# Kernel optimization log

Measured on AMD Instinct MI355X. Metric: run time of the kernel, lower is better.

## Reference

```python
import jax, jax.numpy as jnp
import numpy as np

TOP_K = 4
NORM_TOPK_PROB = True


def setup_inputs() -> dict:
    key = jax.random.key(0)
    kx, kg, k1, k3, k2 = jax.random.split(key, 5)
    B, S, H, I, E = 1, 2048, 1024, 512, 16
    scale = 0.02
    return {
        "hidden_states": jax.random.normal(kx, (B, S, H), jnp.float32),
        "gate_w": jax.random.normal(kg, (E, H), jnp.float32) * scale,   # router Linear weight [E,H]
        "w1": jax.random.normal(k1, (E, I, H), jnp.float32) * scale,    # intermediateDense per expert
        "w3": jax.random.normal(k3, (E, I, H), jnp.float32) * scale,    # intermediateDense2 per expert
        "w2": jax.random.normal(k2, (E, H, I), jnp.float32) * scale,    # outputDense per expert
    }


def reference(hidden_states, gate_w, w1, w3, w2):
    B, S, H = hidden_states.shape
    x = hidden_states.reshape(-1, H)                    # [T,H]
    T = x.shape[0]
    E = gate_w.shape[0]

    # Router: softmax in fp32, top-k, optional renorm (norm_topk_prob=True)
    router_logits = x @ gate_w.T                        # [T,E]
    probs = jax.nn.softmax(router_logits.astype(jnp.float32), axis=-1)
    routing_weights, selected = jax.lax.top_k(probs, TOP_K)   # [T,K], [T,K]
    if NORM_TOPK_PROB:
        routing_weights = routing_weights / routing_weights.sum(-1, keepdims=True)
    routing_weights = routing_weights.astype(x.dtype)

    # Dense per-token expert-weight matrix: zero for unselected experts, so
    # the combine below computes exactly the torch gather->FFN->index_add math.
    w = jnp.zeros((T, E), x.dtype).at[jnp.arange(T)[:, None], selected].add(routing_weights)

    # Gated SiLU FFN for every expert, combined with routing weights.
    h1 = jnp.einsum('th,eih->tei', x, w1)               # [T,E,I]
    h3 = jnp.einsum('th,eih->tei', x, w3)               # [T,E,I]
    act = jax.nn.silu(h1) * h3                          # [T,E,I]
    out = jnp.einsum('tei,ehi,te->th', act, w2, w)      # [T,H]
    return out.reshape(B, S, H)
```

## Files before the change

### kernel.cpp

```cpp
#include <hip/hip_runtime.h>
#include <hip/hip_bf16.h>

#define T 2048
#define H 1024
#define IDIM 512
#define E 16
#define TOPK 4
#define NPAIR (T * TOPK)

typedef short bf16x8 __attribute__((ext_vector_type(8)));
typedef float f32x4 __attribute__((ext_vector_type(4)));

static __device__ __forceinline__ unsigned short f2bf(float f) {
    union { float f; unsigned int u; } v; v.f = f;
    unsigned int r = (v.u + 0x7FFFu + ((v.u >> 16) & 1u)) >> 16;
    return (unsigned short)r;
}
static __device__ __forceinline__ float bf2f(unsigned short s) {
    union { unsigned int u; float f; } v; v.u = ((unsigned int)s) << 16;
    return v.f;
}

static __device__ __forceinline__ void async_ld16(const unsigned short* g, unsigned short* l) {
    __builtin_amdgcn_global_load_lds((const __attribute__((address_space(1))) void*)g,
                                     (__attribute__((address_space(3))) void*)l, 16, 0, 0);
}

__global__ __launch_bounds__(256) void cvt3_kernel(
    const float* __restrict__ w1, const float* __restrict__ w3, const float* __restrict__ w2,
    unsigned short* __restrict__ d1, unsigned short* __restrict__ d3, unsigned short* __restrict__ d2)
{
    const int n4 = (E * IDIM * H) / 4;
    int region = blockIdx.x >> 11;
    int bid = blockIdx.x & 2047;
    const float* src = (region == 0) ? w1 : (region == 1) ? w3 : w2;
    unsigned short* dst = (region == 0) ? d1 : (region == 1) ? d3 : d2;
    int i = bid * 256 + threadIdx.x;
    const int stride = 2048 * 256;
#pragma unroll 4
    for (; i < n4; i += stride) {
        float4 v = ((const float4*)src)[i];
        ushort4 o;
        o.x = f2bf(v.x); o.y = f2bf(v.y); o.z = f2bf(v.z); o.w = f2bf(v.w);
        ((ushort4*)dst)[i] = o;
    }
}

__global__ __launch_bounds__(256) void router_kernel(
    const float* __restrict__ x, const float* __restrict__ gw,
    int* __restrict__ topk_idx, float* __restrict__ topk_w,
    unsigned short* __restrict__ xb)
{
    int tok = blockIdx.x * 4 + (threadIdx.x >> 6);
    int lane = threadIdx.x & 63;
    if (tok >= T) return;
    const float4* xt4 = (const float4*)(x + (size_t)tok * H);
    float4 xr[4];
#pragma unroll
    for (int j = 0; j < 4; ++j) xr[j] = xt4[lane + j * 64];
    ushort4* xbt = (ushort4*)(xb + (size_t)tok * H);
#pragma unroll
    for (int j = 0; j < 4; ++j) {
        ushort4 o;
        o.x = f2bf(xr[j].x); o.y = f2bf(xr[j].y);
        o.z = f2bf(xr[j].z); o.w = f2bf(xr[j].w);
        xbt[lane + j * 64] = o;
    }
    float logits[E];
#pragma unroll
    for (int e = 0; e < E; ++e) {
        const float4* ge4 = (const float4*)(gw + (size_t)e * H);
        float acc = 0.f;
#pragma unroll
        for (int j = 0; j < 4; ++j) {
            float4 g = ge4[lane + j * 64];
            acc += xr[j].x * g.x + xr[j].y * g.y + xr[j].z * g.z + xr[j].w * g.w;
        }
#pragma unroll
        for (int off = 32; off; off >>= 1) acc += __shfl_xor(acc, off, 64);
        logits[e] = acc;
    }
    if (lane == 0) {
        float m = logits[0];
#pragma unroll
        for (int e = 1; e < E; ++e) m = fmaxf(m, logits[e]);
        float p[E];
#pragma unroll
        for (int e = 0; e < E; ++e) p[e] = __expf(logits[e] - m);
        int sel[TOPK]; float wv[TOPK]; float tot = 0.f;
#pragma unroll
        for (int k = 0; k < TOPK; ++k) {
            int best = 0; float bv = -1.f;
#pragma unroll
            for (int e = 0; e < E; ++e) { if (p[e] > bv) { bv = p[e]; best = e; } }
            sel[k] = best; wv[k] = bv; tot += bv; p[best] = -2.f;
        }
#pragma unroll
        for (int k = 0; k < TOPK; ++k) {
            topk_idx[tok * TOPK + k] = sel[k];
            topk_w[tok * TOPK + k] = wv[k] / tot;
        }
    }
}

__global__ __launch_bounds__(256) void hist_kernel(
    const int* __restrict__ topk_idx, int* __restrict__ offsets)
{
    __shared__ int h[4][E];
    int tid = threadIdx.x, wave = tid >> 6;
    if (tid < 4 * E) ((int*)h)[tid] = 0;
    __syncthreads();
    for (int i = tid; i < NPAIR; i += 256) atomicAdd(&h[wave][topk_idx[i]], 1);
    __syncthreads();
    if (tid == 0) {
        int s = 0;
#pragma unroll
        for (int e = 0; e < E; ++e) {
            offsets[e] = s;
            s += h[0][e] + h[1][e] + h[2][e] + h[3][e];
        }
        offsets[E] = s;
    }
}

__global__ __launch_bounds__(256) void scatter_kernel(
    const int* __restrict__ topk_idx,
    const int* __restrict__ offsets, int* __restrict__ cursor,
    int* __restrict__ pair_token, int* __restrict__ inv_pos)
{
    __shared__ int lh[E];
    __shared__ int base[E];
    int tid = threadIdx.x;
    int i = blockIdx.x * 256 + tid;
    if (tid < E) lh[tid] = 0;
    __syncthreads();
    int e = topk_idx[i];
    int lr = atomicAdd(&lh[e], 1);
    __syncthreads();
    if (tid < E) base[tid] = atomicAdd(&cursor[tid], lh[tid]);
    __syncthreads();
    int pos = offsets[e] + base[e] + lr;
    pair_token[pos] = i >> 2;
    inv_pos[i] = pos;
}


__global__ __launch_bounds__(256, 5) void gemm_a_kernel(
    const unsigned short* __restrict__ xb,
    const unsigned short* __restrict__ wb1,
    const unsigned short* __restrict__ wb3,
    const int* __restrict__ offsets,
    const int* __restrict__ pair_token,
    unsigned short* __restrict__ act)
{
    __shared__ unsigned short Xs[2][128 * 32];
    __shared__ unsigned short W1s[2][64 * 32];
    __shared__ unsigned short W3s[2][64 * 32];

    int bid = blockIdx.x;
    int xcd = bid & 7, s0 = bid >> 3;
    int yz = xcd * 16 + (s0 >> 4);
    int e = yz >> 3;
    int n0 = (yz & 7) * 64;
    int t0 = (s0 & 15) * 128;

    int beg = offsets[e];
    int cnt = offsets[e + 1] - beg;
    if (t0 >= cnt) return;

    int tid = threadIdx.x;
    int wave = tid >> 6, lane = tid & 63;

    const unsigned short* xg[2];
#pragma unroll
    for (int i = 0; i < 2; ++i) {
        int slot = wave * 128 + i * 64 + lane;
        int g = slot >> 3, sp = (slot & 7) ^ (g & 7);
        int row = g * 2 + (sp >> 2), c = sp & 3;
        int r = t0 + row; if (r >= cnt) r = cnt - 1;
        xg[i] = xb + (size_t)pair_token[beg + r] * H + c * 8;
    }
    const unsigned short* w1g;
    const unsigned short* w3g;
    {
        int slot = wave * 64 + lane;
        int g = slot >> 3, sp = (slot & 7) ^ (g & 7);
        int row = g * 2 + (sp >> 2), c = sp & 3;
        size_t off = (size_t)e * IDIM * H + (size_t)(n0 + row) * H + c * 8;
        w1g = wb1 + off;
        w3g = wb3 + off;
    }

    int wr = wave >> 1, wc = wave & 1;
    int lm = lane & 15, lq = lane >> 4;

    f32x4 acc1[4][2], acc3[4][2];
#pragma unroll
    for (int mi = 0; mi < 4; ++mi)
#pragma unroll
        for (int nj = 0; nj < 2; ++nj) {
            acc1[mi][nj] = (f32x4){0.f, 0.f, 0.f, 0.f};
            acc3[mi][nj] = (f32x4){0.f, 0.f, 0.f, 0.f};
        }

    int aoff[4], boff[2];
#pragma unroll
    for (int mi = 0; mi < 4; ++mi) {
        int m = wr * 64 + mi * 16 + lm;
        int g = m >> 1;
        aoff[mi] = g * 64 + (((lq + ((m & 1) << 2)) ^ (g & 7)) << 3);
    }
#pragma unroll
    for (int nj = 0; nj < 2; ++nj) {
        int n = wc * 32 + nj * 16 + lm;
        int g = n >> 1;
        boff[nj] = g * 64 + (((lq + ((n & 1) << 2)) ^ (g & 7)) << 3);
    }

#pragma unroll
    for (int i = 0; i < 2; ++i) async_ld16(xg[i], &Xs[0][(wave * 128 + i * 64) * 8]);
    async_ld16(w1g, &W1s[0][wave * 512]);
    async_ld16(w3g, &W3s[0][wave * 512]);

    const int NK = H / 32;
    for (int kk = 0; kk < NK; ++kk) {
        int cur = kk & 1;
        __syncthreads();
        if (kk + 1 < NK) {
            int nxt = cur ^ 1;
            int k1 = (kk + 1) * 32;
#pragma unroll
            for (int i = 0; i < 2; ++i) async_ld16(xg[i] + k1, &Xs[nxt][(wave * 128 + i * 64) * 8]);
            async_ld16(w1g + k1, &W1s[nxt][wave * 512]);
            async_ld16(w3g + k1, &W3s[nxt][wave * 512]);
        }
        bf16x8 af[4], b1[2], b3[2];
#pragma unroll
        for (int mi = 0; mi < 4; ++mi) af[mi] = *(const bf16x8*)&Xs[cur][aoff[mi]];
#pragma unroll
        for (int nj = 0; nj < 2; ++nj) {
            b1[nj] = *(const bf16x8*)&W1s[cur][boff[nj]];
            b3[nj] = *(const bf16x8*)&W3s[cur][boff[nj]];
        }
#pragma unroll
        for (int mi = 0; mi < 4; ++mi)
#pragma unroll
            for (int nj = 0; nj < 2; ++nj) {
                acc1[mi][nj] = __builtin_amdgcn_mfma_f32_16x16x32_bf16(af[mi], b1[nj], acc1[mi][nj], 0, 0, 0);
                acc3[mi][nj] = __builtin_amdgcn_mfma_f32_16x16x32_bf16(af[mi], b3[nj], acc3[mi][nj], 0, 0, 0);
            }
    }
#pragma unroll
    for (int mi = 0; mi < 4; ++mi) {
#pragma unroll
        for (int r = 0; r < 4; ++r) {
            int trow = t0 + wr * 64 + mi * 16 + lq * 4 + r;
            if (trow < cnt) {
                size_t base = (size_t)(beg + trow) * IDIM + n0 + wc * 32 + lm;
#pragma unroll
                for (int nj = 0; nj < 2; ++nj) {
                    float h1 = acc1[mi][nj][r];
                    float sg = h1 / (1.f + __expf(-h1));
                    act[base + nj * 16] = f2bf(sg * acc3[mi][nj][r]);
                }
            }
        }
    }
}

__global__ __launch_bounds__(256, 5) void gemm_b_kernel(
    const unsigned short* __restrict__ act,
    const unsigned short* __restrict__ wb2,
    const int* __restrict__ offsets,
    unsigned short* __restrict__ outp)
{
    __shared__ unsigned short As[2][128 * 32];
    __shared__ unsigned short W2s[2][64 * 32];

    int bid = blockIdx.x;
    int xcd = bid & 7, s0 = bid >> 3;
    int yz = xcd * 32 + (s0 >> 4);
    int e = yz >> 4;
    int h0 = (yz & 15) * 64;
    int t0 = (s0 & 15) * 128;

    int beg = offsets[e];
    int cnt = offsets[e + 1] - beg;
    if (t0 >= cnt) return;

    int tid = threadIdx.x;
    int wave = tid >> 6, lane = tid & 63;

    const unsigned short* ag[2];
#pragma unroll
    for (int i = 0; i < 2; ++i) {
        int slot = wave * 128 + i * 64 + lane;
        int g = slot >> 3, sp = (slot & 7) ^ (g & 7);
        int row = g * 2 + (sp >> 2), c = sp & 3;
        int ar = beg + t0 + row; if (ar > NPAIR - 1) ar = NPAIR - 1;
        ag[i] = act + (size_t)ar * IDIM + c * 8;
    }
    const unsigned short* w2g;
    {
        int slot = wave * 64 + lane;
        int g = slot >> 3, sp = (slot & 7) ^ (g & 7);
        int row = g * 2 + (sp >> 2), c = sp & 3;
        w2g = wb2 + (size_t)e * H * IDIM + (size_t)(h0 + row) * IDIM + c * 8;
    }

    int wr = wave >> 1, wc = wave & 1;
    int lm = lane & 15, lq = lane >> 4;

    f32x4 acc[4][2];
#pragma unroll
    for (int mi = 0; mi < 4; ++mi)
#pragma unroll
        for (int nj = 0; nj < 2; ++nj) acc[mi][nj] = (f32x4){0.f, 0.f, 0.f, 0.f};

    int aoff[4], boff[2];
#pragma unroll
    for (int mi = 0; mi < 4; ++mi) {
        int m = wr * 64 + mi * 16 + lm;
        int g = m >> 1;
        aoff[mi] = g * 64 + (((lq + ((m & 1) << 2)) ^ (g & 7)) << 3);
    }
#pragma unroll
    for (int nj = 0; nj < 2; ++nj) {
        int n = wc * 32 + nj * 16 + lm;
        int g = n >> 1;
        boff[nj] = g * 64 + (((lq + ((n & 1) << 2)) ^ (g & 7)) << 3);
    }

#pragma unroll
    for (int i = 0; i < 2; ++i) async_ld16(ag[i], &As[0][(wave * 128 + i * 64) * 8]);
    async_ld16(w2g, &W2s[0][wave * 512]);

    const int NK = IDIM / 32;
    for (int kk = 0; kk < NK; ++kk) {
        int cur = kk & 1;
        __syncthreads();
        if (kk + 1 < NK) {
            int nxt = cur ^ 1;
            int k1 = (kk + 1) * 32;
#pragma unroll
            for (int i = 0; i < 2; ++i) async_ld16(ag[i] + k1, &As[nxt][(wave * 128 + i * 64) * 8]);
            async_ld16(w2g + k1, &W2s[nxt][wave * 512]);
        }
        bf16x8 af[4], bfr[2];
#pragma unroll
        for (int mi = 0; mi < 4; ++mi) af[mi] = *(const bf16x8*)&As[cur][aoff[mi]];
#pragma unroll
        for (int nj = 0; nj < 2; ++nj) bfr[nj] = *(const bf16x8*)&W2s[cur][boff[nj]];
#pragma unroll
        for (int mi = 0; mi < 4; ++mi)
#pragma unroll
            for (int nj = 0; nj < 2; ++nj)
                acc[mi][nj] = __builtin_amdgcn_mfma_f32_16x16x32_bf16(af[mi], bfr[nj], acc[mi][nj], 0, 0, 0);
    }
#pragma unroll
    for (int mi = 0; mi < 4; ++mi) {
#pragma unroll
        for (int r = 0; r < 4; ++r) {
            int trow = t0 + wr * 64 + mi * 16 + lq * 4 + r;
            if (trow < cnt) {
                unsigned short* orow = outp + (size_t)(beg + trow) * H + h0 + wc * 32 + lm;
#pragma unroll
                for (int nj = 0; nj < 2; ++nj) orow[nj * 16] = f2bf(acc[mi][nj][r]);
            }
        }
    }
}

__global__ __launch_bounds__(256) void combine_kernel(
    const unsigned short* __restrict__ outp, const int* __restrict__ inv_pos,
    const float* __restrict__ topk_w, float* __restrict__ out)
{
    int gid = blockIdx.x * 256 + threadIdx.x;
    int t = gid >> 8;
    int c4 = gid & 255;
    float4 a = make_float4(0.f, 0.f, 0.f, 0.f);
#pragma unroll
    for (int k = 0; k < TOPK; ++k) {
        int pos = inv_pos[t * TOPK + k];
        float w = topk_w[t * TOPK + k];
        ushort4 v = ((const ushort4*)(outp + (size_t)pos * H))[c4];
        a.x += w * bf2f(v.x); a.y += w * bf2f(v.y);
        a.z += w * bf2f(v.z); a.w += w * bf2f(v.w);
    }
    *(float4*)(out + (size_t)t * H + c4 * 4) = a;
}

extern "C" void kernel_launch(void* const* d_in, const int* in_sizes, int n_in,
                              void* d_out, int out_size, void* d_ws, size_t ws_size,
                              hipStream_t stream)
{
    const float* x  = (const float*)d_in[0];
    const float* gw = (const float*)d_in[1];
    const float* w1 = (const float*)d_in[2];
    const float* w3 = (const float*)d_in[3];
    const float* w2 = (const float*)d_in[4];
    float* out = (float*)d_out;

    char* ws = (char*)d_ws;
    int*   cursor     = (int*)(ws + 64);
    int*   offsets    = (int*)(ws + 128);
    int*   topk_idx   = (int*)(ws + 1024);
    float* topk_w     = (float*)(ws + 33792);
    int*   pair_token = (int*)(ws + 66560);
    int*   inv_pos    = (int*)(ws + 99328);
    unsigned short* xb  = (unsigned short*)(ws + 262144);
    unsigned short* wb1 = (unsigned short*)(ws + 8388608);
    unsigned short* wb3 = (unsigned short*)(ws + 25165824);
    unsigned short* wb2 = (unsigned short*)(ws + 41943040);
    unsigned short* act = (unsigned short*)(ws + 58720256);
    unsigned short* outp = (unsigned short*)(ws + 8388608);

    hipMemsetAsync(ws, 0, 256, stream);

    router_kernel<<<T / 4, 256, 0, stream>>>(x, gw, topk_idx, topk_w, xb);
    hist_kernel<<<1, 256, 0, stream>>>(topk_idx, offsets);
    scatter_kernel<<<NPAIR / 256, 256, 0, stream>>>(topk_idx, offsets, cursor,
                                                    pair_token, inv_pos);

    cvt3_kernel<<<3 * 2048, 256, 0, stream>>>(w1, w3, w2, wb1, wb3, wb2);

    gemm_a_kernel<<<2048, 256, 0, stream>>>(xb, wb1, wb3, offsets, pair_token, act);
    gemm_b_kernel<<<4096, 256, 0, stream>>>(act, wb2, offsets, outp);
    combine_kernel<<<(T * H / 4) / 256, 256, 0, stream>>>(outp, inv_pos, topk_w, out);
}
```

Measured before the change: 229.6 us.

## Deepen async LDS prefetch pipelines in both expert GEMM kernels

Replaces the double-buffered k-loop in gemm_a with a 4-stage ring (three tiles in flight) and gemm_b with a 3-stage ring, using explicit vmcnt waits plus raw s_barrier instead of __syncthreads. This keeps more global_load_lds transfers outstanding so load latency is hidden behind MFMA work. The price is more LDS per block, and the occupancy hints drop to 2 blocks/SM for gemm_a and 4 for gemm_b. Correctness depends on the hand-counted vmcnt values matching the number of loads each stage issues.

Result: slower. 234.8 us (+2.2%).

```diff
diff --git a/kernel.cpp b/kernel.cpp
--- a/kernel.cpp
+++ b/kernel.cpp
@@ -145,7 +145,28 @@
 }
 
 
-__global__ __launch_bounds__(256, 5) void gemm_a_kernel(
+static __device__ __forceinline__ void ga_compute(
+    const unsigned short* xs, const unsigned short* w1s, const unsigned short* w3s,
+    const int* aoff, const int* boff, f32x4 acc1[4][2], f32x4 acc3[4][2])
+{
+    bf16x8 af[4], b1[2], b3[2];
+#pragma unroll
+    for (int mi = 0; mi < 4; ++mi) af[mi] = *(const bf16x8*)&xs[aoff[mi]];
+#pragma unroll
+    for (int nj = 0; nj < 2; ++nj) {
+        b1[nj] = *(const bf16x8*)&w1s[boff[nj]];
+        b3[nj] = *(const bf16x8*)&w3s[boff[nj]];
+    }
+#pragma unroll
+    for (int mi = 0; mi < 4; ++mi)
+#pragma unroll
+        for (int nj = 0; nj < 2; ++nj) {
+            acc1[mi][nj] = __builtin_amdgcn_mfma_f32_16x16x32_bf16(af[mi], b1[nj], acc1[mi][nj], 0, 0, 0);
+            acc3[mi][nj] = __builtin_amdgcn_mfma_f32_16x16x32_bf16(af[mi], b3[nj], acc3[mi][nj], 0, 0, 0);
+        }
+}
+
+__global__ __launch_bounds__(256, 2) void gemm_a_kernel(
     const unsigned short* __restrict__ xb,
     const unsigned short* __restrict__ wb1,
     const unsigned short* __restrict__ wb3,
@@ -153,9 +174,9 @@
     const int* __restrict__ pair_token,
     unsigned short* __restrict__ act)
 {
-    __shared__ unsigned short Xs[2][128 * 32];
-    __shared__ unsigned short W1s[2][64 * 32];
-    __shared__ unsigned short W3s[2][64 * 32];
+    __shared__ unsigned short Xs[4][128 * 32];
+    __shared__ unsigned short W1s[4][64 * 32];
+    __shared__ unsigned short W3s[4][64 * 32];
 
     int bid = blockIdx.x;
     int xcd = bid & 7, s0 = bid >> 3;
@@ -217,39 +238,41 @@
         boff[nj] = g * 64 + (((lq + ((n & 1) << 2)) ^ (g & 7)) << 3);
     }
 
-#pragma unroll
-    for (int i = 0; i < 2; ++i) async_ld16(xg[i], &Xs[0][(wave * 128 + i * 64) * 8]);
-    async_ld16(w1g, &W1s[0][wave * 512]);
-    async_ld16(w3g, &W3s[0][wave * 512]);
+    auto stage = [&](int buf, int kt) {
+        int k1 = kt * 32;
+#pragma unroll
+        for (int i = 0; i < 2; ++i)
+            async_ld16(xg[i] + k1, &Xs[buf][(wave * 128 + i * 64) * 8]);
+        async_ld16(w1g + k1, &W1s[buf][wave * 512]);
+        async_ld16(w3g + k1, &W3s[buf][wave * 512]);
+    };
+
+    stage(0, 0); stage(1, 1); stage(2, 2);
 
     const int NK = H / 32;
-    for (int kk = 0; kk < NK; ++kk) {
-        int cur = kk & 1;
-        __syncthreads();
-        if (kk + 1 < NK) {
-            int nxt = cur ^ 1;
-            int k1 = (kk + 1) * 32;
-#pragma unroll
-            for (int i = 0; i < 2; ++i) async_ld16(xg[i] + k1, &Xs[nxt][(wave * 128 + i * 64) * 8]);
-            async_ld16(w1g + k1, &W1s[nxt][wave * 512]);
-            async_ld16(w3g + k1, &W3s[nxt][wave * 512]);
-        }
-        bf16x8 af[4], b1[2], b3[2];
-#pragma unroll
-        for (int mi = 0; mi < 4; ++mi) af[mi] = *(const bf16x8*)&Xs[cur][aoff[mi]];
-#pragma unroll
-        for (int nj = 0; nj < 2; ++nj) {
-            b1[nj] = *(const bf16x8*)&W1s[cur][boff[nj]];
-            b3[nj] = *(const bf16x8*)&W3s[cur][boff[nj]];
-        }
-#pragma unroll
-        for (int mi = 0; mi < 4; ++mi)
-#pragma unroll
-            for (int nj = 0; nj < 2; ++nj) {
-                acc1[mi][nj] = __builtin_amdgcn_mfma_f32_16x16x32_bf16(af[mi], b1[nj], acc1[mi][nj], 0, 0, 0);
-                acc3[mi][nj] = __builtin_amdgcn_mfma_f32_16x16x32_bf16(af[mi], b3[nj], acc3[mi][nj], 0, 0, 0);
-            }
-    }
+    for (int kk = 0; kk < NK - 2; ++kk) {
+        int cur = kk & 3;
+        asm volatile("s_waitcnt vmcnt(8)" ::: "memory");
+        __builtin_amdgcn_s_barrier();
+        __builtin_amdgcn_sched_barrier(0);
+        if (kk + 3 < NK) stage((kk + 3) & 3, kk + 3);
+        ga_compute(Xs[cur], W1s[cur], W3s[cur], aoff, boff, acc1, acc3);
+    }
+    {
+        int cur = (NK - 2) & 3;
+        asm volatile("s_waitcnt vmcnt(4)" ::: "memory");
+        __builtin_amdgcn_s_barrier();
+        __builtin_amdgcn_sched_barrier(0);
+        ga_compute(Xs[cur], W1s[cur], W3s[cur], aoff, boff, acc1, acc3);
+    }
+    {
+        int cur = (NK - 1) & 3;
+        asm volatile("s_waitcnt vmcnt(0)" ::: "memory");
+        __builtin_amdgcn_s_barrier();
+        __builtin_amdgcn_sched_barrier(0);
+        ga_compute(Xs[cur], W1s[cur], W3s[cur], aoff, boff, acc1, acc3);
+    }
+
 #pragma unroll
     for (int mi = 0; mi < 4; ++mi) {
 #pragma unroll
@@ -268,14 +291,30 @@
     }
 }
 
-__global__ __launch_bounds__(256, 5) void gemm_b_kernel(
+static __device__ __forceinline__ void gb_compute(
+    const unsigned short* as, const unsigned short* w2s,
+    const int* aoff, const int* boff, f32x4 acc[4][2])
+{
+    bf16x8 af[4], bfr[2];
+#pragma unroll
+    for (int mi = 0; mi < 4; ++mi) af[mi] = *(const bf16x8*)&as[aoff[mi]];
+#pragma unroll
+    for (int nj = 0; nj < 2; ++nj) bfr[nj] = *(const bf16x8*)&w2s[boff[nj]];
+#pragma unroll
+    for (int mi = 0; mi < 4; ++mi)
+#pragma unroll
+        for (int nj = 0; nj < 2; ++nj)
+            acc[mi][nj] = __builtin_amdgcn_mfma_f32_16x16x32_bf16(af[mi], bfr[nj], acc[mi][nj], 0, 0, 0);
+}
+
+__global__ __launch_bounds__(256, 4) void gemm_b_kernel(
     const unsigned short* __restrict__ act,
     const unsigned short* __restrict__ wb2,
     const int* __restrict__ offsets,
     unsigned short* __restrict__ outp)
 {
-    __shared__ unsigned short As[2][128 * 32];
-    __shared__ unsigned short W2s[2][64 * 32];
+    __shared__ unsigned short As[3][128 * 32];
+    __shared__ unsigned short W2s[3][64 * 32];
 
     int bid = blockIdx.x;
     int xcd = bid & 7, s0 = bid >> 3;
@@ -331,32 +370,34 @@
         boff[nj] = g * 64 + (((lq + ((n & 1) << 2)) ^ (g & 7)) << 3);
     }
 
-#pragma unroll
-    for (int i = 0; i < 2; ++i) async_ld16(ag[i], &As[0][(wave * 128 + i * 64) * 8]);
-    async_ld16(w2g, &W2s[0][wave * 512]);
+    auto stage = [&](int buf, int kt) {
+        int k1 = kt * 32;
+#pragma unroll
+        for (int i = 0; i < 2; ++i)
+            async_ld16(ag[i] + k1, &As[buf][(wave * 128 + i * 64) * 8]);
+        async_ld16(w2g + k1, &W2s[buf][wave * 512]);
+    };
+
+    stage(0, 0); stage(1, 1);
 
     const int NK = IDIM / 32;
-    for (int kk = 0; kk < NK; ++kk) {
-        int cur = kk & 1;
-        __syncthreads();
-        if (kk + 1 < NK) {
-            int nxt = cur ^ 1;
-            int k1 = (kk + 1) * 32;
-#pragma unroll
-            for (int i = 0; i < 2; ++i) async_ld16(ag[i] + k1, &As[nxt][(wave * 128 + i * 64) * 8]);
-            async_ld16(w2g + k1, &W2s[nxt][wave * 512]);
-        }
-        bf16x8 af[4], bfr[2];
-#pragma unroll
-        for (int mi = 0; mi < 4; ++mi) af[mi] = *(const bf16x8*)&As[cur][aoff[mi]];
-#pragma unroll
-        for (int nj = 0; nj < 2; ++nj) bfr[nj] = *(const bf16x8*)&W2s[cur][boff[nj]];
-#pragma unroll
-        for (int mi = 0; mi < 4; ++mi)
-#pragma unroll
-            for (int nj = 0; nj < 2; ++nj)
-                acc[mi][nj] = __builtin_amdgcn_mfma_f32_16x16x32_bf16(af[mi], bfr[nj], acc[mi][nj], 0, 0, 0);
-    }
+    int cur = 0, pre = 2;
+    for (int kk = 0; kk < NK - 1; ++kk) {
+        asm volatile("s_waitcnt vmcnt(3)" ::: "memory");
+        __builtin_amdgcn_s_barrier();
+        __builtin_amdgcn_sched_barrier(0);
+        if (kk + 2 < NK) stage(pre, kk + 2);
+        gb_compute(As[cur], W2s[cur], aoff, boff, acc);
+        cur = (cur == 2) ? 0 : cur + 1;
+        pre = (pre == 2) ? 0 : pre + 1;
+    }
+    {
+        asm volatile("s_waitcnt vmcnt(0)" ::: "memory");
+        __builtin_amdgcn_s_barrier();
+        __builtin_amdgcn_sched_barrier(0);
+        gb_compute(As[cur], W2s[cur], aoff, boff, acc);
+    }
+
 #pragma unroll
     for (int mi = 0; mi < 4; ++mi) {
 #pragma unroll
```

## Fuse weight conversion with router, fold histogram, scatter-add output in GEMM B

Applied to the files above, without the earlier changes.

Merges the weight-conversion and router kernels into one launch and builds the expert histogram with global atomics inside the router, leaving a tiny scan kernel in place of the histogram kernel. GEMM B now multiplies by the routing weight and atomically adds fp32 results straight into the zeroed output, which removes the bf16 intermediate buffer and the combine kernel. The cost is an extra memset of the output and contended fp32 atomics, up to four per output element, plus non-deterministic summation order.

Result: slower. 328.4 us (+43.0%).

```diff
diff --git a/kernel.cpp b/kernel.cpp
--- a/kernel.cpp
+++ b/kernel.cpp
@@ -26,32 +26,32 @@
                                      (__attribute__((address_space(3))) void*)l, 16, 0, 0);
 }
 
-__global__ __launch_bounds__(256) void cvt3_kernel(
+__global__ __launch_bounds__(256) void prep_kernel(
     const float* __restrict__ w1, const float* __restrict__ w3, const float* __restrict__ w2,
-    unsigned short* __restrict__ d1, unsigned short* __restrict__ d3, unsigned short* __restrict__ d2)
-{
-    const int n4 = (E * IDIM * H) / 4;
-    int region = blockIdx.x >> 11;
-    int bid = blockIdx.x & 2047;
-    const float* src = (region == 0) ? w1 : (region == 1) ? w3 : w2;
-    unsigned short* dst = (region == 0) ? d1 : (region == 1) ? d3 : d2;
-    int i = bid * 256 + threadIdx.x;
-    const int stride = 2048 * 256;
-#pragma unroll 4
-    for (; i < n4; i += stride) {
-        float4 v = ((const float4*)src)[i];
-        ushort4 o;
-        o.x = f2bf(v.x); o.y = f2bf(v.y); o.z = f2bf(v.z); o.w = f2bf(v.w);
-        ((ushort4*)dst)[i] = o;
-    }
-}
-
-__global__ __launch_bounds__(256) void router_kernel(
+    unsigned short* __restrict__ d1, unsigned short* __restrict__ d3, unsigned short* __restrict__ d2,
     const float* __restrict__ x, const float* __restrict__ gw,
     int* __restrict__ topk_idx, float* __restrict__ topk_w,
-    unsigned short* __restrict__ xb)
-{
-    int tok = blockIdx.x * 4 + (threadIdx.x >> 6);
+    unsigned short* __restrict__ xb, int* __restrict__ ghist)
+{
+    if (blockIdx.x < 3 * 2048) {
+        const int n4 = (E * IDIM * H) / 4;
+        int region = blockIdx.x >> 11;
+        int bid = blockIdx.x & 2047;
+        const float* src = (region == 0) ? w1 : (region == 1) ? w3 : w2;
+        unsigned short* dst = (region == 0) ? d1 : (region == 1) ? d3 : d2;
+        int i = bid * 256 + threadIdx.x;
+        const int stride = 2048 * 256;
+#pragma unroll 4
+        for (; i < n4; i += stride) {
+            float4 v = ((const float4*)src)[i];
+            ushort4 o;
+            o.x = f2bf(v.x); o.y = f2bf(v.y); o.z = f2bf(v.z); o.w = f2bf(v.w);
+            ((ushort4*)dst)[i] = o;
+        }
+        return;
+    }
+    int rbid = blockIdx.x - 3 * 2048;
+    int tok = rbid * 4 + (threadIdx.x >> 6);
     int lane = threadIdx.x & 63;
     if (tok >= T) return;
     const float4* xt4 = (const float4*)(x + (size_t)tok * H);
@@ -99,34 +99,26 @@
         for (int k = 0; k < TOPK; ++k) {
             topk_idx[tok * TOPK + k] = sel[k];
             topk_w[tok * TOPK + k] = wv[k] / tot;
-        }
-    }
-}
-
-__global__ __launch_bounds__(256) void hist_kernel(
-    const int* __restrict__ topk_idx, int* __restrict__ offsets)
-{
-    __shared__ int h[4][E];
-    int tid = threadIdx.x, wave = tid >> 6;
-    if (tid < 4 * E) ((int*)h)[tid] = 0;
-    __syncthreads();
-    for (int i = tid; i < NPAIR; i += 256) atomicAdd(&h[wave][topk_idx[i]], 1);
-    __syncthreads();
-    if (tid == 0) {
+            atomicAdd(&ghist[sel[k]], 1);
+        }
+    }
+}
+
+__global__ __launch_bounds__(64) void scan_kernel(
+    const int* __restrict__ ghist, int* __restrict__ offsets)
+{
+    if (threadIdx.x == 0) {
         int s = 0;
 #pragma unroll
-        for (int e = 0; e < E; ++e) {
-            offsets[e] = s;
-            s += h[0][e] + h[1][e] + h[2][e] + h[3][e];
-        }
+        for (int e = 0; e < E; ++e) { offsets[e] = s; s += ghist[e]; }
         offsets[E] = s;
     }
 }
 
 __global__ __launch_bounds__(256) void scatter_kernel(
-    const int* __restrict__ topk_idx,
+    const int* __restrict__ topk_idx, const float* __restrict__ topk_w,
     const int* __restrict__ offsets, int* __restrict__ cursor,
-    int* __restrict__ pair_token, int* __restrict__ inv_pos)
+    int* __restrict__ pair_token, float* __restrict__ pair_w)
 {
     __shared__ int lh[E];
     __shared__ int base[E];
@@ -141,7 +133,7 @@
     __syncthreads();
     int pos = offsets[e] + base[e] + lr;
     pair_token[pos] = i >> 2;
-    inv_pos[i] = pos;
+    pair_w[pos] = topk_w[i];
 }
 
 
@@ -272,7 +264,9 @@
     const unsigned short* __restrict__ act,
     const unsigned short* __restrict__ wb2,
     const int* __restrict__ offsets,
-    unsigned short* __restrict__ outp)
+    const int* __restrict__ pair_token,
+    const float* __restrict__ pair_w,
+    float* __restrict__ out)
 {
     __shared__ unsigned short As[2][128 * 32];
     __shared__ unsigned short W2s[2][64 * 32];
@@ -363,31 +357,15 @@
         for (int r = 0; r < 4; ++r) {
             int trow = t0 + wr * 64 + mi * 16 + lq * 4 + r;
             if (trow < cnt) {
-                unsigned short* orow = outp + (size_t)(beg + trow) * H + h0 + wc * 32 + lm;
-#pragma unroll
-                for (int nj = 0; nj < 2; ++nj) orow[nj * 16] = f2bf(acc[mi][nj][r]);
+                int p = beg + trow;
+                int tok = pair_token[p];
+                float wgt = pair_w[p];
+                float* orow = out + (size_t)tok * H + h0 + wc * 32 + lm;
+                atomicAdd(&orow[0],  wgt * acc[mi][0][r]);
+                atomicAdd(&orow[16], wgt * acc[mi][1][r]);
             }
         }
     }
-}
-
-__global__ __launch_bounds__(256) void combine_kernel(
-    const unsigned short* __restrict__ outp, const int* __restrict__ inv_pos,
-    const float* __restrict__ topk_w, float* __restrict__ out)
-{
-    int gid = blockIdx.x * 256 + threadIdx.x;
-    int t = gid >> 8;
-    int c4 = gid & 255;
-    float4 a = make_float4(0.f, 0.f, 0.f, 0.f);
-#pragma unroll
-    for (int k = 0; k < TOPK; ++k) {
-        int pos = inv_pos[t * TOPK + k];
-        float w = topk_w[t * TOPK + k];
-        ushort4 v = ((const ushort4*)(outp + (size_t)pos * H))[c4];
-        a.x += w * bf2f(v.x); a.y += w * bf2f(v.y);
-        a.z += w * bf2f(v.z); a.w += w * bf2f(v.w);
-    }
-    *(float4*)(out + (size_t)t * H + c4 * 4) = a;
 }
 
 extern "C" void kernel_launch(void* const* d_in, const int* in_sizes, int n_in,
@@ -402,29 +380,28 @@
     float* out = (float*)d_out;
 
     char* ws = (char*)d_ws;
+    int*   ghist      = (int*)(ws + 0);
     int*   cursor     = (int*)(ws + 64);
     int*   offsets    = (int*)(ws + 128);
     int*   topk_idx   = (int*)(ws + 1024);
     float* topk_w     = (float*)(ws + 33792);
     int*   pair_token = (int*)(ws + 66560);
-    int*   inv_pos    = (int*)(ws + 99328);
+    float* pair_w     = (float*)(ws + 99328);
     unsigned short* xb  = (unsigned short*)(ws + 262144);
     unsigned short* wb1 = (unsigned short*)(ws + 8388608);
     unsigned short* wb3 = (unsigned short*)(ws + 25165824);
     unsigned short* wb2 = (unsigned short*)(ws + 41943040);
     unsigned short* act = (unsigned short*)(ws + 58720256);
-    unsigned short* outp = (unsigned short*)(ws + 8388608);
 
     hipMemsetAsync(ws, 0, 256, stream);
-
-    router_kernel<<<T / 4, 256, 0, stream>>>(x, gw, topk_idx, topk_w, xb);
-    hist_kernel<<<1, 256, 0, stream>>>(topk_idx, offsets);
-    scatter_kernel<<<NPAIR / 256, 256, 0, stream>>>(topk_idx, offsets, cursor,
-                                                    pair_token, inv_pos);
-
-    cvt3_kernel<<<3 * 2048, 256, 0, stream>>>(w1, w3, w2, wb1, wb3, wb2);
+    hipMemsetAsync(out, 0, (size_t)T * H * sizeof(float), stream);
+
+    prep_kernel<<<3 * 2048 + T / 4, 256, 0, stream>>>(
+        w1, w3, w2, wb1, wb3, wb2, x, gw, topk_idx, topk_w, xb, ghist);
+    scan_kernel<<<1, 64, 0, stream>>>(ghist, offsets);
+    scatter_kernel<<<NPAIR / 256, 256, 0, stream>>>(topk_idx, topk_w, offsets, cursor,
+                                                    pair_token, pair_w);
 
     gemm_a_kernel<<<2048, 256, 0, stream>>>(xb, wb1, wb3, offsets, pair_token, act);
-    gemm_b_kernel<<<4096, 256, 0, stream>>>(act, wb2, offsets, outp);
-    combine_kernel<<<(T * H / 4) / 256, 256, 0, stream>>>(outp, inv_pos, topk_w, out);
-}
+    gemm_b_kernel<<<4096, 256, 0, stream>>>(act, wb2, offsets, pair_token, pair_w, out);
+}
```

## Fuse fp32-to-bf16 weight conversion into expert GEMM tile loads

Applied to the files above, without the earlier changes.

Drops the separate kernel that converted all expert weights to bf16 in workspace. Both expert GEMMs now read fp32 weights straight from global memory into registers, convert them to bf16 and write them to LDS, prefetching one k-tile ahead. The token tile shrinks from 128 to 64 rows and the grids double, with occupancy hints adjusted. This removes a full pass of weight read and write traffic, but each expert's fp32 weights are now re-read by more token tiles at twice the bytes, and the synchronous register staging replaces the asynchronous global-to-LDS path for the weights.

Result: slower. 248.8 us (+8.4%).

```diff
diff --git a/kernel.cpp b/kernel.cpp
--- a/kernel.cpp
+++ b/kernel.cpp
@@ -24,26 +24,6 @@
 static __device__ __forceinline__ void async_ld16(const unsigned short* g, unsigned short* l) {
     __builtin_amdgcn_global_load_lds((const __attribute__((address_space(1))) void*)g,
                                      (__attribute__((address_space(3))) void*)l, 16, 0, 0);
-}
-
-__global__ __launch_bounds__(256) void cvt3_kernel(
-    const float* __restrict__ w1, const float* __restrict__ w3, const float* __restrict__ w2,
-    unsigned short* __restrict__ d1, unsigned short* __restrict__ d3, unsigned short* __restrict__ d2)
-{
-    const int n4 = (E * IDIM * H) / 4;
-    int region = blockIdx.x >> 11;
-    int bid = blockIdx.x & 2047;
-    const float* src = (region == 0) ? w1 : (region == 1) ? w3 : w2;
-    unsigned short* dst = (region == 0) ? d1 : (region == 1) ? d3 : d2;
-    int i = bid * 256 + threadIdx.x;
-    const int stride = 2048 * 256;
-#pragma unroll 4
-    for (; i < n4; i += stride) {
-        float4 v = ((const float4*)src)[i];
-        ushort4 o;
-        o.x = f2bf(v.x); o.y = f2bf(v.y); o.z = f2bf(v.z); o.w = f2bf(v.w);
-        ((ushort4*)dst)[i] = o;
-    }
 }
 
 __global__ __launch_bounds__(256) void router_kernel(
@@ -145,24 +125,24 @@
 }
 
 
-__global__ __launch_bounds__(256, 5) void gemm_a_kernel(
+__global__ __launch_bounds__(256, 4) void gemm_a_kernel(
     const unsigned short* __restrict__ xb,
-    const unsigned short* __restrict__ wb1,
-    const unsigned short* __restrict__ wb3,
+    const float* __restrict__ w1,
+    const float* __restrict__ w3,
     const int* __restrict__ offsets,
     const int* __restrict__ pair_token,
     unsigned short* __restrict__ act)
 {
-    __shared__ unsigned short Xs[2][128 * 32];
+    __shared__ unsigned short Xs[2][64 * 32];
     __shared__ unsigned short W1s[2][64 * 32];
     __shared__ unsigned short W3s[2][64 * 32];
 
     int bid = blockIdx.x;
     int xcd = bid & 7, s0 = bid >> 3;
-    int yz = xcd * 16 + (s0 >> 4);
+    int yz = xcd * 16 + (s0 >> 5);
     int e = yz >> 3;
     int n0 = (yz & 7) * 64;
-    int t0 = (s0 & 15) * 128;
+    int t0 = (s0 & 31) * 64;
 
     int beg = offsets[e];
     int cnt = offsets[e + 1] - beg;
@@ -171,42 +151,31 @@
     int tid = threadIdx.x;
     int wave = tid >> 6, lane = tid & 63;
 
-    const unsigned short* xg[2];
-#pragma unroll
-    for (int i = 0; i < 2; ++i) {
-        int slot = wave * 128 + i * 64 + lane;
-        int g = slot >> 3, sp = (slot & 7) ^ (g & 7);
-        int row = g * 2 + (sp >> 2), c = sp & 3;
-        int r = t0 + row; if (r >= cnt) r = cnt - 1;
-        xg[i] = xb + (size_t)pair_token[beg + r] * H + c * 8;
-    }
-    const unsigned short* w1g;
-    const unsigned short* w3g;
-    {
-        int slot = wave * 64 + lane;
-        int g = slot >> 3, sp = (slot & 7) ^ (g & 7);
-        int row = g * 2 + (sp >> 2), c = sp & 3;
-        size_t off = (size_t)e * IDIM * H + (size_t)(n0 + row) * H + c * 8;
-        w1g = wb1 + off;
-        w3g = wb3 + off;
-    }
+    int sg = tid >> 3, sp = (tid & 7) ^ (sg & 7);
+    int srow = sg * 2 + (sp >> 2), sc = sp & 3;
+
+    int r = t0 + srow; if (r >= cnt) r = cnt - 1;
+    const unsigned short* xg = xb + (size_t)pair_token[beg + r] * H + sc * 8;
+
+    const float* w1g = w1 + (size_t)e * IDIM * H + (size_t)(n0 + srow) * H + sc * 8;
+    const float* w3g = w3 + (size_t)e * IDIM * H + (size_t)(n0 + srow) * H + sc * 8;
 
     int wr = wave >> 1, wc = wave & 1;
     int lm = lane & 15, lq = lane >> 4;
 
-    f32x4 acc1[4][2], acc3[4][2];
-#pragma unroll
-    for (int mi = 0; mi < 4; ++mi)
+    f32x4 acc1[2][2], acc3[2][2];
+#pragma unroll
+    for (int mi = 0; mi < 2; ++mi)
 #pragma unroll
         for (int nj = 0; nj < 2; ++nj) {
             acc1[mi][nj] = (f32x4){0.f, 0.f, 0.f, 0.f};
             acc3[mi][nj] = (f32x4){0.f, 0.f, 0.f, 0.f};
         }
 
-    int aoff[4], boff[2];
-#pragma unroll
-    for (int mi = 0; mi < 4; ++mi) {
-        int m = wr * 64 + mi * 16 + lm;
+    int aoff[2], boff[2];
+#pragma unroll
+    for (int mi = 0; mi < 2; ++mi) {
+        int m = wr * 32 + mi * 16 + lm;
         int g = m >> 1;
         aoff[mi] = g * 64 + (((lq + ((m & 1) << 2)) ^ (g & 7)) << 3);
     }
@@ -217,10 +186,34 @@
         boff[nj] = g * 64 + (((lq + ((n & 1) << 2)) ^ (g & 7)) << 3);
     }
 
-#pragma unroll
-    for (int i = 0; i < 2; ++i) async_ld16(xg[i], &Xs[0][(wave * 128 + i * 64) * 8]);
-    async_ld16(w1g, &W1s[0][wave * 512]);
-    async_ld16(w3g, &W3s[0][wave * 512]);
+    float4 ra0, ra1, rb0, rb1;
+    auto wload = [&](int kt, float4& a0, float4& a1, float4& b0, float4& b1) {
+        const float* p1 = w1g + kt * 32;
+        const float* p3 = w3g + kt * 32;
+        a0 = *(const float4*)p1; a1 = *(const float4*)(p1 + 4);
+        b0 = *(const float4*)p3; b1 = *(const float4*)(p3 + 4);
+    };
+    auto wwrite = [&](int buf, float4 a0, float4 a1, float4 b0, float4 b1) {
+        bf16x8 v1, v3;
+        v1[0] = (short)f2bf(a0.x); v1[1] = (short)f2bf(a0.y);
+        v1[2] = (short)f2bf(a0.z); v1[3] = (short)f2bf(a0.w);
+        v1[4] = (short)f2bf(a1.x); v1[5] = (short)f2bf(a1.y);
+        v1[6] = (short)f2bf(a1.z); v1[7] = (short)f2bf(a1.w);
+        v3[0] = (short)f2bf(b0.x); v3[1] = (short)f2bf(b0.y);
+        v3[2] = (short)f2bf(b0.z); v3[3] = (short)f2bf(b0.w);
+        v3[4] = (short)f2bf(b1.x); v3[5] = (short)f2bf(b1.y);
+        v3[6] = (short)f2bf(b1.z); v3[7] = (short)f2bf(b1.w);
+        *(bf16x8*)&W1s[buf][tid * 8] = v1;
+        *(bf16x8*)&W3s[buf][tid * 8] = v3;
+    };
+
+    {
+        float4 ca0, ca1, cb0, cb1;
+        wload(0, ca0, ca1, cb0, cb1);
+        async_ld16(xg, &Xs[0][tid * 8]);
+        wwrite(0, ca0, ca1, cb0, cb1);
+    }
+    wload(1, ra0, ra1, rb0, rb1);
 
     const int NK = H / 32;
     for (int kk = 0; kk < NK; ++kk) {
@@ -228,61 +221,59 @@
         __syncthreads();
         if (kk + 1 < NK) {
             int nxt = cur ^ 1;
-            int k1 = (kk + 1) * 32;
-#pragma unroll
-            for (int i = 0; i < 2; ++i) async_ld16(xg[i] + k1, &Xs[nxt][(wave * 128 + i * 64) * 8]);
-            async_ld16(w1g + k1, &W1s[nxt][wave * 512]);
-            async_ld16(w3g + k1, &W3s[nxt][wave * 512]);
-        }
-        bf16x8 af[4], b1[2], b3[2];
-#pragma unroll
-        for (int mi = 0; mi < 4; ++mi) af[mi] = *(const bf16x8*)&Xs[cur][aoff[mi]];
+            async_ld16(xg + (kk + 1) * 32, &Xs[nxt][tid * 8]);
+            wwrite(nxt, ra0, ra1, rb0, rb1);
+            if (kk + 2 < NK) wload(kk + 2, ra0, ra1, rb0, rb1);
+        }
+        bf16x8 af[2], b1f[2], b3f[2];
+#pragma unroll
+        for (int mi = 0; mi < 2; ++mi) af[mi] = *(const bf16x8*)&Xs[cur][aoff[mi]];
 #pragma unroll
         for (int nj = 0; nj < 2; ++nj) {
-            b1[nj] = *(const bf16x8*)&W1s[cur][boff[nj]];
-            b3[nj] = *(const bf16x8*)&W3s[cur][boff[nj]];
-        }
-#pragma unroll
-        for (int mi = 0; mi < 4; ++mi)
+            b1f[nj] = *(const bf16x8*)&W1s[cur][boff[nj]];
+            b3f[nj] = *(const bf16x8*)&W3s[cur][boff[nj]];
+        }
+#pragma unroll
+        for (int mi = 0; mi < 2; ++mi)
 #pragma unroll
             for (int nj = 0; nj < 2; ++nj) {
-                acc1[mi][nj] = __builtin_amdgcn_mfma_f32_16x16x32_bf16(af[mi], b1[nj], acc1[mi][nj], 0, 0, 0);
-                acc3[mi][nj] = __builtin_amdgcn_mfma_f32_16x16x32_bf16(af[mi], b3[nj], acc3[mi][nj], 0, 0, 0);
+                acc1[mi][nj] = __builtin_amdgcn_mfma_f32_16x16x32_bf16(af[mi], b1f[nj], acc1[mi][nj], 0, 0, 0);
+                acc3[mi][nj] = __builtin_amdgcn_mfma_f32_16x16x32_bf16(af[mi], b3f[nj], acc3[mi][nj], 0, 0, 0);
             }
     }
 #pragma unroll
-    for (int mi = 0; mi < 4; ++mi) {
-#pragma unroll
-        for (int r = 0; r < 4; ++r) {
-            int trow = t0 + wr * 64 + mi * 16 + lq * 4 + r;
+    for (int mi = 0; mi < 2; ++mi) {
+#pragma unroll
+        for (int rr = 0; rr < 4; ++rr) {
+            int trow = t0 + wr * 32 + mi * 16 + lq * 4 + rr;
             if (trow < cnt) {
                 size_t base = (size_t)(beg + trow) * IDIM + n0 + wc * 32 + lm;
 #pragma unroll
                 for (int nj = 0; nj < 2; ++nj) {
-                    float h1 = acc1[mi][nj][r];
+                    float h1 = acc1[mi][nj][rr];
                     float sg = h1 / (1.f + __expf(-h1));
-                    act[base + nj * 16] = f2bf(sg * acc3[mi][nj][r]);
+                    act[base + nj * 16] = f2bf(sg * acc3[mi][nj][rr]);
                 }
             }
         }
     }
 }
 
-__global__ __launch_bounds__(256, 5) void gemm_b_kernel(
+__global__ __launch_bounds__(256, 6) void gemm_b_kernel(
     const unsigned short* __restrict__ act,
-    const unsigned short* __restrict__ wb2,
+    const float* __restrict__ w2,
     const int* __restrict__ offsets,
     unsigned short* __restrict__ outp)
 {
-    __shared__ unsigned short As[2][128 * 32];
+    __shared__ unsigned short As[2][64 * 32];
     __shared__ unsigned short W2s[2][64 * 32];
 
     int bid = blockIdx.x;
     int xcd = bid & 7, s0 = bid >> 3;
-    int yz = xcd * 32 + (s0 >> 4);
+    int yz = xcd * 32 + (s0 >> 5);
     int e = yz >> 4;
     int h0 = (yz & 15) * 64;
-    int t0 = (s0 & 15) * 128;
+    int t0 = (s0 & 31) * 64;
 
     int beg = offsets[e];
     int cnt = offsets[e + 1] - beg;
@@ -291,36 +282,26 @@
     int tid = threadIdx.x;
     int wave = tid >> 6, lane = tid & 63;
 
-    const unsigned short* ag[2];
-#pragma unroll
-    for (int i = 0; i < 2; ++i) {
-        int slot = wave * 128 + i * 64 + lane;
-        int g = slot >> 3, sp = (slot & 7) ^ (g & 7);
-        int row = g * 2 + (sp >> 2), c = sp & 3;
-        int ar = beg + t0 + row; if (ar > NPAIR - 1) ar = NPAIR - 1;
-        ag[i] = act + (size_t)ar * IDIM + c * 8;
-    }
-    const unsigned short* w2g;
-    {
-        int slot = wave * 64 + lane;
-        int g = slot >> 3, sp = (slot & 7) ^ (g & 7);
-        int row = g * 2 + (sp >> 2), c = sp & 3;
-        w2g = wb2 + (size_t)e * H * IDIM + (size_t)(h0 + row) * IDIM + c * 8;
-    }
+    int sg = tid >> 3, sp = (tid & 7) ^ (sg & 7);
+    int srow = sg * 2 + (sp >> 2), sc = sp & 3;
+
+    int ar = beg + t0 + srow; if (ar > NPAIR - 1) ar = NPAIR - 1;
+    const unsigned short* ag = act + (size_t)ar * IDIM + sc * 8;
+    const float* w2g = w2 + (size_t)e * H * IDIM + (size_t)(h0 + srow) * IDIM + sc * 8;
 
     int wr = wave >> 1, wc = wave & 1;
     int lm = lane & 15, lq = lane >> 4;
 
-    f32x4 acc[4][2];
-#pragma unroll
-    for (int mi = 0; mi < 4; ++mi)
+    f32x4 acc[2][2];
+#pragma unroll
+    for (int mi = 0; mi < 2; ++mi)
 #pragma unroll
         for (int nj = 0; nj < 2; ++nj) acc[mi][nj] = (f32x4){0.f, 0.f, 0.f, 0.f};
 
-    int aoff[4], boff[2];
-#pragma unroll
-    for (int mi = 0; mi < 4; ++mi) {
-        int m = wr * 64 + mi * 16 + lm;
+    int aoff[2], boff[2];
+#pragma unroll
+    for (int mi = 0; mi < 2; ++mi) {
+        int m = wr * 32 + mi * 16 + lm;
         int g = m >> 1;
         aoff[mi] = g * 64 + (((lq + ((m & 1) << 2)) ^ (g & 7)) << 3);
     }
@@ -331,9 +312,27 @@
         boff[nj] = g * 64 + (((lq + ((n & 1) << 2)) ^ (g & 7)) << 3);
     }
 
-#pragma unroll
-    for (int i = 0; i < 2; ++i) async_ld16(ag[i], &As[0][(wave * 128 + i * 64) * 8]);
-    async_ld16(w2g, &W2s[0][wave * 512]);
+    float4 ra0, ra1;
+    auto wload = [&](int kt, float4& a0, float4& a1) {
+        const float* p = w2g + kt * 32;
+        a0 = *(const float4*)p; a1 = *(const float4*)(p + 4);
+    };
+    auto wwrite = [&](int buf, float4 a0, float4 a1) {
+        bf16x8 v;
+        v[0] = (short)f2bf(a0.x); v[1] = (short)f2bf(a0.y);
+        v[2] = (short)f2bf(a0.z); v[3] = (short)f2bf(a0.w);
+        v[4] = (short)f2bf(a1.x); v[5] = (short)f2bf(a1.y);
+        v[6] = (short)f2bf(a1.z); v[7] = (short)f2bf(a1.w);
+        *(bf16x8*)&W2s[buf][tid * 8] = v;
+    };
+
+    {
+        float4 ca0, ca1;
+        wload(0, ca0, ca1);
+        async_ld16(ag, &As[0][tid * 8]);
+        wwrite(0, ca0, ca1);
+    }
+    wload(1, ra0, ra1);
 
     const int NK = IDIM / 32;
     for (int kk = 0; kk < NK; ++kk) {
@@ -341,31 +340,30 @@
         __syncthreads();
         if (kk + 1 < NK) {
             int nxt = cur ^ 1;
-            int k1 = (kk + 1) * 32;
-#pragma unroll
-            for (int i = 0; i < 2; ++i) async_ld16(ag[i] + k1, &As[nxt][(wave * 128 + i * 64) * 8]);
-            async_ld16(w2g + k1, &W2s[nxt][wave * 512]);
-        }
-        bf16x8 af[4], bfr[2];
-#pragma unroll
-        for (int mi = 0; mi < 4; ++mi) af[mi] = *(const bf16x8*)&As[cur][aoff[mi]];
-#pragma unroll
-        for (int nj = 0; nj < 2; ++nj) bfr[nj] = *(const bf16x8*)&W2s[cur][boff[nj]];
-#pragma unroll
-        for (int mi = 0; mi < 4; ++mi)
+            async_ld16(ag + (kk + 1) * 32, &As[nxt][tid * 8]);
+            wwrite(nxt, ra0, ra1);
+            if (kk + 2 < NK) wload(kk + 2, ra0, ra1);
+        }
+        bf16x8 af[2], bf[2];
+#pragma unroll
+        for (int mi = 0; mi < 2; ++mi) af[mi] = *(const bf16x8*)&As[cur][aoff[mi]];
+#pragma unroll
+        for (int nj = 0; nj < 2; ++nj) bf[nj] = *(const bf16x8*)&W2s[cur][boff[nj]];
+#pragma unroll
+        for (int mi = 0; mi < 2; ++mi)
 #pragma unroll
             for (int nj = 0; nj < 2; ++nj)
-                acc[mi][nj] = __builtin_amdgcn_mfma_f32_16x16x32_bf16(af[mi], bfr[nj], acc[mi][nj], 0, 0, 0);
-    }
-#pragma unroll
-    for (int mi = 0; mi < 4; ++mi) {
-#pragma unroll
-        for (int r = 0; r < 4; ++r) {
-            int trow = t0 + wr * 64 + mi * 16 + lq * 4 + r;
+                acc[mi][nj] = __builtin_amdgcn_mfma_f32_16x16x32_bf16(af[mi], bf[nj], acc[mi][nj], 0, 0, 0);
+    }
+#pragma unroll
+    for (int mi = 0; mi < 2; ++mi) {
+#pragma unroll
+        for (int rr = 0; rr < 4; ++rr) {
+            int trow = t0 + wr * 32 + mi * 16 + lq * 4 + rr;
             if (trow < cnt) {
                 unsigned short* orow = outp + (size_t)(beg + trow) * H + h0 + wc * 32 + lm;
 #pragma unroll
-                for (int nj = 0; nj < 2; ++nj) orow[nj * 16] = f2bf(acc[mi][nj][r]);
+                for (int nj = 0; nj < 2; ++nj) orow[nj * 16] = f2bf(acc[mi][nj][rr]);
             }
         }
     }
@@ -408,12 +406,9 @@
     float* topk_w     = (float*)(ws + 33792);
     int*   pair_token = (int*)(ws + 66560);
     int*   inv_pos    = (int*)(ws + 99328);
-    unsigned short* xb  = (unsigned short*)(ws + 262144);
-    unsigned short* wb1 = (unsigned short*)(ws + 8388608);
-    unsigned short* wb3 = (unsigned short*)(ws + 25165824);
-    unsigned short* wb2 = (unsigned short*)(ws + 41943040);
-    unsigned short* act = (unsigned short*)(ws + 58720256);
-    unsigned short* outp = (unsigned short*)(ws + 8388608);
+    unsigned short* xb   = (unsigned short*)(ws + 262144);
+    unsigned short* act  = (unsigned short*)(ws + 8388608);
+    unsigned short* outp = (unsigned short*)(ws + 25165824);
 
     hipMemsetAsync(ws, 0, 256, stream);
 
@@ -422,9 +417,7 @@
     scatter_kernel<<<NPAIR / 256, 256, 0, stream>>>(topk_idx, offsets, cursor,
                                                     pair_token, inv_pos);
 
-    cvt3_kernel<<<3 * 2048, 256, 0, stream>>>(w1, w3, w2, wb1, wb3, wb2);
-
-    gemm_a_kernel<<<2048, 256, 0, stream>>>(xb, wb1, wb3, offsets, pair_token, act);
-    gemm_b_kernel<<<4096, 256, 0, stream>>>(act, wb2, offsets, outp);
+    gemm_a_kernel<<<4096, 256, 0, stream>>>(xb, w1, w3, offsets, pair_token, act);
+    gemm_b_kernel<<<8192, 256, 0, stream>>>(act, w2, offsets, outp);
     combine_kernel<<<(T * H / 4) / 256, 256, 0, stream>>>(outp, inv_pos, topk_w, out);
 }
```
